# Optimization experiments

Hardware: AMD Instinct MI355X
Metric: run time of the kernel (lower is better)

The kernel has to match this reference:

```python
import jax, jax.numpy as jnp
import numpy as np

B, N, C = 2, 1024, 81          # images, proposals/img, classes (class 0 = background)
H, W = 1024, 1024              # image size
D = 100                        # detections_per_img
WX, WY, WW, WH = 10.0, 10.0, 5.0, 5.0   # BoxCoder weights
SCORE_THRESH = 0.05
NMS_THRESH = 0.5
BBOX_XFORM_CLIP = float(np.log(1000.0 / 16.0))
NEG = -1e30
TO_REMOVE = 1.0


def setup_inputs() -> dict:
    key = jax.random.key(0)
    k1, k2, k3, k4 = jax.random.split(key, 4)
    class_logits = jax.random.normal(k1, (B, N, C), jnp.float32)
    regression_outputs = jax.random.normal(k2, (B, N, C * 4), jnp.float32) * 0.5
    # build valid xyxy proposal boxes inside the image
    cxy = jax.random.uniform(k3, (B, N, 2), jnp.float32, 0.0, W - 1.0)
    wh = jax.random.uniform(k4, (B, N, 2), jnp.float32, 8.0, 256.0)
    x1y1 = jnp.clip(cxy - wh / 2, 0.0, W - 1.0)
    x2y2 = jnp.clip(cxy + wh / 2, 0.0, W - 1.0)
    proposals = jnp.concatenate([x1y1, x2y2], axis=-1)
    return dict(class_logits=class_logits,
                regression_outputs=regression_outputs,
                proposals=proposals)


def decode(rel, props):
    # rel: [N, C, 4], props: [N, 4] xyxy -> decoded per-class boxes [N, C, 4], clipped to image
    widths = props[:, 2] - props[:, 0] + TO_REMOVE   # [N]
    heights = props[:, 3] - props[:, 1] + TO_REMOVE
    ctr_x = props[:, 0] + 0.5 * widths
    ctr_y = props[:, 1] + 0.5 * heights
    dx = rel[..., 0] / WX
    dy = rel[..., 1] / WY
    dw = jnp.minimum(rel[..., 2] / WW, BBOX_XFORM_CLIP)
    dh = jnp.minimum(rel[..., 3] / WH, BBOX_XFORM_CLIP)
    pcx = dx * widths[:, None] + ctr_x[:, None]
    pcy = dy * heights[:, None] + ctr_y[:, None]
    pw = jnp.exp(dw) * widths[:, None]
    ph = jnp.exp(dh) * heights[:, None]
    x1 = pcx - 0.5 * pw
    y1 = pcy - 0.5 * ph
    x2 = pcx + 0.5 * pw - 1.0
    y2 = pcy + 0.5 * ph - 1.0
    # clip_to_image
    x1 = jnp.clip(x1, 0.0, W - TO_REMOVE)
    y1 = jnp.clip(y1, 0.0, H - TO_REMOVE)
    x2 = jnp.clip(x2, 0.0, W - TO_REMOVE)
    y2 = jnp.clip(y2, 0.0, H - TO_REMOVE)
    return jnp.stack([x1, y1, x2, y2], axis=-1)


def pairwise_iou(b):
    # b: [N, 4] -> [N, N]
    area = (b[:, 2] - b[:, 0] + TO_REMOVE) * (b[:, 3] - b[:, 1] + TO_REMOVE)
    lt = jnp.maximum(b[:, None, :2], b[None, :, :2])
    rb = jnp.minimum(b[:, None, 2:], b[None, :, 2:])
    wh = jnp.clip(rb - lt + TO_REMOVE, 0.0)
    inter = wh[..., 0] * wh[..., 1]
    return inter / (area[:, None] + area[None, :] - inter)


def nms_keep(boxes, scores):
    # boxes [N,4], scores [N] (NEG for below-threshold boxes) -> keep mask [N] bool
    order = jnp.argsort(-scores)
    b = boxes[order]
    iou = pairwise_iou(b)                       # [N, N]
    valid = scores[order] > NEG / 2             # below-threshold boxes never participate
    idx = jnp.arange(N)

    def body(i, keep):
        sup = keep[i] & (iou[i] > NMS_THRESH) & (idx > i)
        return keep & ~sup

    keep_sorted = jax.lax.fori_loop(0, N, body, valid)
    return jnp.zeros(N, bool).at[order].set(keep_sorted)


def _per_image(logits, rel, props):
    probs = jax.nn.softmax(logits, axis=-1)                 # [N, C]
    boxes = decode(rel.reshape(N, C, 4), props)             # [N, C, 4]
    cls_boxes = jnp.transpose(boxes[:, 1:, :], (1, 0, 2))   # [C-1, N, 4]  (skip background)
    cls_scores = probs[:, 1:].T                              # [C-1, N]
    valid = cls_scores > SCORE_THRESH
    masked_in = jnp.where(valid, cls_scores, NEG)
    keep = jax.vmap(nms_keep)(cls_boxes, masked_in)          # [C-1, N]
    surv = jnp.where(keep & valid, cls_scores, NEG)
    top_scores, top_idx = jax.lax.top_k(surv.reshape(-1), D)  # over (C-1)*N candidates
    cls_idx = top_idx // N
    box_idx = top_idx % N
    sel_boxes = cls_boxes[cls_idx, box_idx]                  # [D, 4]
    labels = cls_idx + 1
    ok = top_scores > NEG / 2
    return (jnp.where(ok[:, None], sel_boxes, 0.0),
            jnp.where(ok, top_scores, 0.0),
            jnp.where(ok, labels, -1))


def reference(class_logits, regression_outputs, proposals):
    # returns (boxes [B,D,4], scores [B,D], labels [B,D]); invalid slots zeroed / label -1
    return jax.vmap(_per_image)(class_logits, regression_outputs, proposals)
```

## Files before the change

kernel.cpp:

```cpp
#include <hip/hip_runtime.h>
#include <math.h>
#include <float.h>

#define BN 2
#define NP 1024
#define NC 81
#define ND 100
#define MAXC 8192
#define CAP 1024
#define NBIN 4096
#define SCORE_T 0.05f
#define NMS_T 0.5f
#define BBOX_CLIP 4.135166556742356f

__device__ __forceinline__ void decode_box(
    const float* __restrict__ props, const float* __restrict__ regress,
    int b, int n, int c, float& x1, float& y1, float& x2, float& y2)
{
    const float* pr = props + ((size_t)b * NP + n) * 4;
    float p0 = pr[0], p1 = pr[1], p2 = pr[2], p3 = pr[3];
    float w  = p2 - p0 + 1.0f, h = p3 - p1 + 1.0f;
    float cx = p0 + 0.5f * w,  cy = p1 + 0.5f * h;
    const float* rl = regress + (((size_t)b * NP + n) * NC + c) * 4;
    float dx = rl[0] / 10.0f, dy = rl[1] / 10.0f;
    float dw = fminf(rl[2] / 5.0f, BBOX_CLIP);
    float dh = fminf(rl[3] / 5.0f, BBOX_CLIP);
    float pcx = dx * w + cx, pcy = dy * h + cy;
    float pw  = expf(dw) * w, ph = expf(dh) * h;
    x1 = pcx - 0.5f * pw; y1 = pcy - 0.5f * ph;
    x2 = pcx + 0.5f * pw - 1.0f; y2 = pcy + 0.5f * ph - 1.0f;
    x1 = fminf(fmaxf(x1, 0.f), 1023.f);
    y1 = fminf(fmaxf(y1, 0.f), 1023.f);
    x2 = fminf(fmaxf(x2, 0.f), 1023.f);
    y2 = fminf(fmaxf(y2, 0.f), 1023.f);
}

__global__ __launch_bounds__(256) void softmax_probs_kernel(
    const float* __restrict__ logits, float* __restrict__ probs_t, int* __restrict__ cnt)
{
    int g = blockIdx.x * 256 + threadIdx.x;
    if (g == 0) { cnt[0] = 0; cnt[1] = 0; }
    if (g >= BN * NP) return;
    int b = g / NP, n = g % NP;
    const float* row = logits + (size_t)g * NC;
    float m = -FLT_MAX;
    for (int i = 0; i < NC; ++i) m = fmaxf(m, row[i]);
    float s = 0.f;
    for (int i = 0; i < NC; ++i) s += expf(row[i] - m);
    for (int c = 1; c < NC; ++c)
        probs_t[((size_t)b * (NC - 1) + (c - 1)) * NP + n] = expf(row[c] - m) / s;
}

__global__ __launch_bounds__(64) void per_class_nms_kernel(
    const float* __restrict__ probs_t, const float* __restrict__ regress,
    const float* __restrict__ props, int* __restrict__ cnt,
    unsigned long long* __restrict__ g_key)
{
    const int b   = blockIdx.x / (NC - 1);
    const int cls = blockIdx.x % (NC - 1);
    const int c   = cls + 1;
    const int tid = threadIdx.x;

    __shared__ float s_score[NP];
    __shared__ int   s_idx[NP];
    __shared__ float s_x1[NP], s_y1[NP], s_x2[NP], s_y2[NP], s_area[NP];
    __shared__ int   s_keep[NP];
    __shared__ int   s_cnt;

    if (tid == 0) s_cnt = 0;
    __syncthreads();

    const float* prow = probs_t + ((size_t)b * (NC - 1) + cls) * NP;
    for (int n = tid; n < NP; n += 64) {
        float p = prow[n];
        if (p > SCORE_T) {
            int k = atomicAdd(&s_cnt, 1);
            s_score[k] = p;
            s_idx[k]   = n;
        }
    }
    __syncthreads();
    const int M = s_cnt;
    if (M == 0) return;

    int Mp = 1; while (Mp < M) Mp <<= 1;
    for (int i = M + tid; i < Mp; i += 64) { s_score[i] = -FLT_MAX; s_idx[i] = NP + i; }
    __syncthreads();

    for (int k = 2; k <= Mp; k <<= 1) {
        for (int j = k >> 1; j > 0; j >>= 1) {
            for (int i = tid; i < Mp; i += 64) {
                int ixj = i ^ j;
                if (ixj > i) {
                    bool desc = ((i & k) == 0);
                    float si = s_score[i], sj = s_score[ixj];
                    if (desc ? (si < sj) : (si > sj)) {
                        s_score[i] = sj; s_score[ixj] = si;
                        int t = s_idx[i]; s_idx[i] = s_idx[ixj]; s_idx[ixj] = t;
                    }
                }
            }
            __syncthreads();
        }
    }

    for (int i = tid; i < M; i += 64) {
        int n = s_idx[i];
        float x1, y1, x2, y2;
        decode_box(props, regress, b, n, c, x1, y1, x2, y2);
        s_x1[i] = x1; s_y1[i] = y1; s_x2[i] = x2; s_y2[i] = y2;
        s_area[i] = (x2 - x1 + 1.f) * (y2 - y1 + 1.f);
        s_keep[i] = 1;
    }
    __syncthreads();

    for (int i = 0; i < M; ++i) {
        if (s_keep[i]) {
            float x1i = s_x1[i], y1i = s_y1[i], x2i = s_x2[i], y2i = s_y2[i], ai = s_area[i];
            for (int j = i + 1 + tid; j < M; j += 64) {
                float lx = fmaxf(x1i, s_x1[j]);
                float ly = fmaxf(y1i, s_y1[j]);
                float rx = fminf(x2i, s_x2[j]);
                float ry = fminf(y2i, s_y2[j]);
                float wd = fmaxf(rx - lx + 1.f, 0.f);
                float ht = fmaxf(ry - ly + 1.f, 0.f);
                float inter = wd * ht;
                float iou = inter / (ai + s_area[j] - inter);
                if (iou > NMS_T) s_keep[j] = 0;
            }
        }
        __syncthreads();
    }

    for (int i = tid; i < M; i += 64) {
        if (s_keep[i]) {
            int pos = atomicAdd(&cnt[b], 1);
            if (pos < MAXC) {
                unsigned int sb = __float_as_uint(s_score[i]);
                unsigned int f  = (unsigned int)(cls * NP + s_idx[i]);
                g_key[(size_t)b * MAXC + pos] =
                    ((unsigned long long)sb << 32) | (unsigned long long)(0xFFFFFFFFu - f);
            }
        }
    }
}

__device__ __forceinline__ void emit_slot(
    float* __restrict__ out, const float* __restrict__ props,
    const float* __restrict__ regress, int b, int d, unsigned long long key)
{
    float score = __uint_as_float((unsigned int)(key >> 32));
    float* ob = out + ((size_t)b * ND + d) * 4;
    float* os = out + (size_t)BN * ND * 4 + b * ND + d;
    float* ol = out + (size_t)BN * ND * 5 + b * ND + d;
    if (score > 0.f) {
        unsigned int f = 0xFFFFFFFFu - (unsigned int)(key & 0xFFFFFFFFu);
        int cls = f / NP, n = f % NP;
        float x1, y1, x2, y2;
        decode_box(props, regress, b, n, cls + 1, x1, y1, x2, y2);
        ob[0] = x1; ob[1] = y1; ob[2] = x2; ob[3] = y2;
        *os = score;
        *ol = (float)(cls + 1);
    } else {
        ob[0] = 0.f; ob[1] = 0.f; ob[2] = 0.f; ob[3] = 0.f;
        *os = 0.f;
        *ol = -1.f;
    }
}

__global__ __launch_bounds__(256) void topk_kernel(
    const int* __restrict__ cnt, unsigned long long* __restrict__ g_key,
    const float* __restrict__ props, const float* __restrict__ regress,
    float* __restrict__ out)
{
    const int b = blockIdx.x;
    const int tid = threadIdx.x;

    __shared__ int hist[NBIN];
    __shared__ unsigned long long cbuf[CAP];
    __shared__ int s_bstar, s_cnt2;

    int K = cnt[b]; if (K > MAXC) K = MAXC;
    const unsigned long long* keys = g_key + (size_t)b * MAXC;

    for (int i = tid; i < NBIN; i += 256) hist[i] = 0;
    if (tid == 0) s_cnt2 = 0;
    __syncthreads();

    for (int i = tid; i < K; i += 256)
        atomicAdd(&hist[(int)(keys[i] >> 52)], 1);
    __syncthreads();

    if (tid < 64) {
        int l = tid;
        int gs = 0;
        for (int q = 0; q < 64; ++q) gs += hist[l * 64 + q];
        int pre = gs;
        for (int off = 1; off < 64; off <<= 1) {
            int v = __shfl_up(pre, off, 64);
            if (l >= off) pre += v;
        }
        int total = __shfl(pre, 63, 64);
        int S = total - pre + gs;
        unsigned long long ball = __ballot(S >= ND);
        int gstar = ball ? (63 - __clzll((long long)ball)) : 0;
        int Sg = __shfl(S, gstar, 64);
        int Gg = __shfl(gs, gstar, 64);
        int A  = Sg - Gg;
        int h  = hist[gstar * 64 + l];
        int pre2 = h;
        for (int off = 1; off < 64; off <<= 1) {
            int v = __shfl_up(pre2, off, 64);
            if (l >= off) pre2 += v;
        }
        int T = Gg - pre2 + h;
        unsigned long long ball2 = __ballot(A + T >= ND);
        int binin = ball2 ? (63 - __clzll((long long)ball2)) : 0;
        if (l == 0) s_bstar = gstar * 64 + binin;
    }
    __syncthreads();
    const int bstar = s_bstar;

    for (int i = tid; i < K; i += 256) {
        unsigned long long key = keys[i];
        if ((int)(key >> 52) >= bstar) {
            int p = atomicAdd(&s_cnt2, 1);
            if (p < CAP) cbuf[p] = key;
        }
    }
    __syncthreads();
    const int Tt = s_cnt2;

    if (Tt <= CAP) {
        int Tp = 128; while (Tp < Tt) Tp <<= 1;
        for (int i = Tt + tid; i < Tp; i += 256) cbuf[i] = 0ull;
        __syncthreads();
        for (int k = 2; k <= Tp; k <<= 1) {
            for (int j = k >> 1; j > 0; j >>= 1) {
                for (int i = tid; i < Tp; i += 256) {
                    int ixj = i ^ j;
                    if (ixj > i) {
                        bool desc = ((i & k) == 0);
                        unsigned long long a = cbuf[i], c2 = cbuf[ixj];
                        if (desc ? (a < c2) : (a > c2)) { cbuf[i] = c2; cbuf[ixj] = a; }
                    }
                }
                __syncthreads();
            }
        }
        for (int d = tid; d < ND; d += 256)
            emit_slot(out, props, regress, b, d, cbuf[d]);
    } else {
        __shared__ unsigned long long rk[256];
        __shared__ int rp[256];
        for (int d = 0; d < ND; ++d) {
            unsigned long long bk = 0ull; int bp = -1;
            for (int t = tid; t < K; t += 256) {
                unsigned long long k2 = g_key[(size_t)b * MAXC + t];
                if (k2 > bk) { bk = k2; bp = t; }
            }
            rk[tid] = bk; rp[tid] = bp;
            __syncthreads();
            for (int off = 128; off > 0; off >>= 1) {
                if (tid < off && rk[tid + off] > rk[tid]) {
                    rk[tid] = rk[tid + off]; rp[tid] = rp[tid + off];
                }
                __syncthreads();
            }
            if (tid == 0) {
                emit_slot(out, props, regress, b, d, rk[0]);
                if (rp[0] >= 0) g_key[(size_t)b * MAXC + rp[0]] = 0ull;
            }
            __syncthreads();
        }
    }
}

extern "C" void kernel_launch(void* const* d_in, const int* in_sizes, int n_in,
                              void* d_out, int out_size, void* d_ws, size_t ws_size,
                              hipStream_t stream) {
    const float* logits  = (const float*)d_in[0];
    const float* regress = (const float*)d_in[1];
    const float* props   = (const float*)d_in[2];
    float* out = (float*)d_out;

    char* ws = (char*)d_ws;
    int*   cnt     = (int*)  (ws);
    float* probs_t = (float*)(ws + 256);
    unsigned long long* g_key = (unsigned long long*)(ws + 256 + (size_t)BN * (NC - 1) * NP * 4);

    hipLaunchKernelGGL(softmax_probs_kernel, dim3((BN * NP + 255) / 256), dim3(256), 0, stream,
                       logits, probs_t, cnt);
    hipLaunchKernelGGL(per_class_nms_kernel, dim3(BN * (NC - 1)), dim3(64), 0, stream,
                       probs_t, regress, props, cnt, g_key);
    hipLaunchKernelGGL(topk_kernel, dim3(BN), dim3(256), 0, stream,
                       cnt, g_key, props, regress, out);
}
```

Baseline: 118.7 us.

## Fuse per-class NMS and top-k via last-block-done pattern, pack sort keys

Merges the NMS and top-k kernels into one launch: each per-class block does its NMS, then increments a per-image done counter, and the last block for each image runs the histogram and top-k selection. The NMS sort now orders packed 64-bit score/index keys instead of separate score and index arrays. Shared memory is unioned between the two phases, and the softmax kernel caches each row in registers with 64-thread blocks. This removes one launch and its gap. It adds a serial top-k tail run by a single 64-thread block, and it truncates candidates per class at 512, which could drop valid boxes if more pass the threshold.

Result: slower. 124.7 us (+5.1%).

```diff
diff --git a/kernel.cpp b/kernel.cpp
--- a/kernel.cpp
+++ b/kernel.cpp
@@ -7,11 +7,14 @@
 #define NC 81
 #define ND 100
 #define MAXC 8192
-#define CAP 1024
+#define CAP2 512
+#define CAPT 512
 #define NBIN 4096
 #define SCORE_T 0.05f
 #define NMS_T 0.5f
 #define BBOX_CLIP 4.135166556742356f
+
+typedef unsigned long long ull;
 
 __device__ __forceinline__ void decode_box(
     const float* __restrict__ props, const float* __restrict__ regress,
@@ -35,119 +38,9 @@
     y2 = fminf(fmaxf(y2, 0.f), 1023.f);
 }
 
-__global__ __launch_bounds__(256) void softmax_probs_kernel(
-    const float* __restrict__ logits, float* __restrict__ probs_t, int* __restrict__ cnt)
-{
-    int g = blockIdx.x * 256 + threadIdx.x;
-    if (g == 0) { cnt[0] = 0; cnt[1] = 0; }
-    if (g >= BN * NP) return;
-    int b = g / NP, n = g % NP;
-    const float* row = logits + (size_t)g * NC;
-    float m = -FLT_MAX;
-    for (int i = 0; i < NC; ++i) m = fmaxf(m, row[i]);
-    float s = 0.f;
-    for (int i = 0; i < NC; ++i) s += expf(row[i] - m);
-    for (int c = 1; c < NC; ++c)
-        probs_t[((size_t)b * (NC - 1) + (c - 1)) * NP + n] = expf(row[c] - m) / s;
-}
-
-__global__ __launch_bounds__(64) void per_class_nms_kernel(
-    const float* __restrict__ probs_t, const float* __restrict__ regress,
-    const float* __restrict__ props, int* __restrict__ cnt,
-    unsigned long long* __restrict__ g_key)
-{
-    const int b   = blockIdx.x / (NC - 1);
-    const int cls = blockIdx.x % (NC - 1);
-    const int c   = cls + 1;
-    const int tid = threadIdx.x;
-
-    __shared__ float s_score[NP];
-    __shared__ int   s_idx[NP];
-    __shared__ float s_x1[NP], s_y1[NP], s_x2[NP], s_y2[NP], s_area[NP];
-    __shared__ int   s_keep[NP];
-    __shared__ int   s_cnt;
-
-    if (tid == 0) s_cnt = 0;
-    __syncthreads();
-
-    const float* prow = probs_t + ((size_t)b * (NC - 1) + cls) * NP;
-    for (int n = tid; n < NP; n += 64) {
-        float p = prow[n];
-        if (p > SCORE_T) {
-            int k = atomicAdd(&s_cnt, 1);
-            s_score[k] = p;
-            s_idx[k]   = n;
-        }
-    }
-    __syncthreads();
-    const int M = s_cnt;
-    if (M == 0) return;
-
-    int Mp = 1; while (Mp < M) Mp <<= 1;
-    for (int i = M + tid; i < Mp; i += 64) { s_score[i] = -FLT_MAX; s_idx[i] = NP + i; }
-    __syncthreads();
-
-    for (int k = 2; k <= Mp; k <<= 1) {
-        for (int j = k >> 1; j > 0; j >>= 1) {
-            for (int i = tid; i < Mp; i += 64) {
-                int ixj = i ^ j;
-                if (ixj > i) {
-                    bool desc = ((i & k) == 0);
-                    float si = s_score[i], sj = s_score[ixj];
-                    if (desc ? (si < sj) : (si > sj)) {
-                        s_score[i] = sj; s_score[ixj] = si;
-                        int t = s_idx[i]; s_idx[i] = s_idx[ixj]; s_idx[ixj] = t;
-                    }
-                }
-            }
-            __syncthreads();
-        }
-    }
-
-    for (int i = tid; i < M; i += 64) {
-        int n = s_idx[i];
-        float x1, y1, x2, y2;
-        decode_box(props, regress, b, n, c, x1, y1, x2, y2);
-        s_x1[i] = x1; s_y1[i] = y1; s_x2[i] = x2; s_y2[i] = y2;
-        s_area[i] = (x2 - x1 + 1.f) * (y2 - y1 + 1.f);
-        s_keep[i] = 1;
-    }
-    __syncthreads();
-
-    for (int i = 0; i < M; ++i) {
-        if (s_keep[i]) {
-            float x1i = s_x1[i], y1i = s_y1[i], x2i = s_x2[i], y2i = s_y2[i], ai = s_area[i];
-            for (int j = i + 1 + tid; j < M; j += 64) {
-                float lx = fmaxf(x1i, s_x1[j]);
-                float ly = fmaxf(y1i, s_y1[j]);
-                float rx = fminf(x2i, s_x2[j]);
-                float ry = fminf(y2i, s_y2[j]);
-                float wd = fmaxf(rx - lx + 1.f, 0.f);
-                float ht = fmaxf(ry - ly + 1.f, 0.f);
-                float inter = wd * ht;
-                float iou = inter / (ai + s_area[j] - inter);
-                if (iou > NMS_T) s_keep[j] = 0;
-            }
-        }
-        __syncthreads();
-    }
-
-    for (int i = tid; i < M; i += 64) {
-        if (s_keep[i]) {
-            int pos = atomicAdd(&cnt[b], 1);
-            if (pos < MAXC) {
-                unsigned int sb = __float_as_uint(s_score[i]);
-                unsigned int f  = (unsigned int)(cls * NP + s_idx[i]);
-                g_key[(size_t)b * MAXC + pos] =
-                    ((unsigned long long)sb << 32) | (unsigned long long)(0xFFFFFFFFu - f);
-            }
-        }
-    }
-}
-
 __device__ __forceinline__ void emit_slot(
     float* __restrict__ out, const float* __restrict__ props,
-    const float* __restrict__ regress, int b, int d, unsigned long long key)
+    const float* __restrict__ regress, int b, int d, ull key)
 {
     float score = __uint_as_float((unsigned int)(key >> 32));
     float* ob = out + ((size_t)b * ND + d) * 4;
@@ -168,33 +61,158 @@
     }
 }
 
-__global__ __launch_bounds__(256) void topk_kernel(
-    const int* __restrict__ cnt, unsigned long long* __restrict__ g_key,
-    const float* __restrict__ props, const float* __restrict__ regress,
-    float* __restrict__ out)
-{
-    const int b = blockIdx.x;
+__device__ __forceinline__ void bitonic_desc(ull* a, int len, int tid, int nthr)
+{
+    for (int k = 2; k <= len; k <<= 1) {
+        for (int j = k >> 1; j > 0; j >>= 1) {
+            for (int i = tid; i < len; i += nthr) {
+                int ixj = i ^ j;
+                if (ixj > i) {
+                    bool desc = ((i & k) == 0);
+                    ull x = a[i], y = a[ixj];
+                    if (desc ? (x < y) : (x > y)) { a[i] = y; a[ixj] = x; }
+                }
+            }
+            __syncthreads();
+        }
+    }
+}
+
+__global__ __launch_bounds__(64) void softmax_probs_kernel(
+    const float* __restrict__ logits, float* __restrict__ probs_t,
+    int* __restrict__ cnt, int* __restrict__ done)
+{
+    int g = blockIdx.x * 64 + threadIdx.x;
+    if (g == 0) { cnt[0] = 0; cnt[1] = 0; done[0] = 0; done[1] = 0; }
+    if (g >= BN * NP) return;
+    int b = g / NP, n = g % NP;
+    const float* row = logits + (size_t)g * NC;
+    float r[NC];
+    #pragma unroll
+    for (int i = 0; i < NC; ++i) r[i] = row[i];
+    float m = -FLT_MAX;
+    #pragma unroll
+    for (int i = 0; i < NC; ++i) m = fmaxf(m, r[i]);
+    float e[NC];
+    float s = 0.f;
+    #pragma unroll
+    for (int i = 0; i < NC; ++i) { e[i] = expf(r[i] - m); s += e[i]; }
+    #pragma unroll
+    for (int c = 1; c < NC; ++c)
+        probs_t[((size_t)b * (NC - 1) + (c - 1)) * NP + n] = e[c] / s;
+}
+
+__global__ __launch_bounds__(64) void nms_topk_kernel(
+    const float* __restrict__ probs_t, const float* __restrict__ regress,
+    const float* __restrict__ props, int* __restrict__ cnt, int* __restrict__ done,
+    ull* __restrict__ g_key, float* __restrict__ out)
+{
     const int tid = threadIdx.x;
-
-    __shared__ int hist[NBIN];
-    __shared__ unsigned long long cbuf[CAP];
-    __shared__ int s_bstar, s_cnt2;
-
-    int K = cnt[b]; if (K > MAXC) K = MAXC;
-    const unsigned long long* keys = g_key + (size_t)b * MAXC;
-
-    for (int i = tid; i < NBIN; i += 256) hist[i] = 0;
+    const int idx = blockIdx.x;
+    const int b   = idx / (NC - 1);
+    const int cls = idx % (NC - 1);
+    const int c   = cls + 1;
+
+    __shared__ union {
+        struct {
+            ull   key[CAP2];
+            float x1[CAP2], y1[CAP2], x2[CAP2], y2[CAP2], area[CAP2];
+            int   keep[CAP2];
+        } a;
+        struct {
+            int hist[NBIN];
+            ull cbuf[CAPT];
+        } t;
+    } sm;
+    __shared__ int s_cnt, s_ret, s_bstar, s_cnt2;
+
+    if (tid == 0) s_cnt = 0;
+    __syncthreads();
+
+    const float* prow = probs_t + ((size_t)b * (NC - 1) + cls) * NP;
+    for (int n = tid; n < NP; n += 64) {
+        float p = prow[n];
+        if (p > SCORE_T) {
+            int k = atomicAdd(&s_cnt, 1);
+            if (k < CAP2)
+                sm.a.key[k] = ((ull)__float_as_uint(p) << 32)
+                            | (ull)(0xFFFFFFFFu - (unsigned)n);
+        }
+    }
+    __syncthreads();
+    int M = s_cnt; if (M > CAP2) M = CAP2;
+
+    if (M > 0) {
+        int Mp = 2; while (Mp < M) Mp <<= 1;
+        for (int i = M + tid; i < Mp; i += 64) sm.a.key[i] = 0ull;
+        __syncthreads();
+
+        bitonic_desc(sm.a.key, Mp, tid, 64);
+
+        for (int i = tid; i < M; i += 64) {
+            int n = (int)(0xFFFFFFFFu - (unsigned)(sm.a.key[i] & 0xFFFFFFFFu));
+            float x1, y1, x2, y2;
+            decode_box(props, regress, b, n, c, x1, y1, x2, y2);
+            sm.a.x1[i] = x1; sm.a.y1[i] = y1; sm.a.x2[i] = x2; sm.a.y2[i] = y2;
+            sm.a.area[i] = (x2 - x1 + 1.f) * (y2 - y1 + 1.f);
+            sm.a.keep[i] = 1;
+        }
+        __syncthreads();
+
+        for (int i = 0; i < M; ++i) {
+            if (sm.a.keep[i]) {
+                float x1i = sm.a.x1[i], y1i = sm.a.y1[i];
+                float x2i = sm.a.x2[i], y2i = sm.a.y2[i], ai = sm.a.area[i];
+                for (int j = i + 1 + tid; j < M; j += 64) {
+                    float lx = fmaxf(x1i, sm.a.x1[j]);
+                    float ly = fmaxf(y1i, sm.a.y1[j]);
+                    float rx = fminf(x2i, sm.a.x2[j]);
+                    float ry = fminf(y2i, sm.a.y2[j]);
+                    float wd = fmaxf(rx - lx + 1.f, 0.f);
+                    float ht = fmaxf(ry - ly + 1.f, 0.f);
+                    float inter = wd * ht;
+                    float iou = inter / (ai + sm.a.area[j] - inter);
+                    if (iou > NMS_T) sm.a.keep[j] = 0;
+                }
+            }
+            __syncthreads();
+        }
+
+        for (int i = tid; i < M; i += 64) {
+            if (sm.a.keep[i]) {
+                int pos = atomicAdd(&cnt[b], 1);
+                if (pos < MAXC) {
+                    ull key = sm.a.key[i];
+                    unsigned n = 0xFFFFFFFFu - (unsigned)(key & 0xFFFFFFFFu);
+                    unsigned f = (unsigned)cls * NP + n;
+                    g_key[(size_t)b * MAXC + pos] =
+                        (key & 0xFFFFFFFF00000000ull) | (ull)(0xFFFFFFFFu - f);
+                }
+            }
+        }
+    }
+
+    __threadfence();
+    if (tid == 0) s_ret = atomicAdd(&done[b], 1);
+    __syncthreads();
+    if (s_ret != (NC - 1) - 1) return;
+    __threadfence();
+
+    int K = atomicAdd(&cnt[b], 0); if (K > MAXC) K = MAXC;
+    ull* keys = g_key + (size_t)b * MAXC;
+
+    for (int i = tid; i < NBIN; i += 64) sm.t.hist[i] = 0;
     if (tid == 0) s_cnt2 = 0;
     __syncthreads();
 
-    for (int i = tid; i < K; i += 256)
-        atomicAdd(&hist[(int)(keys[i] >> 52)], 1);
-    __syncthreads();
-
-    if (tid < 64) {
+    for (int i = tid; i < K; i += 64)
+        atomicAdd(&sm.t.hist[(int)(keys[i] >> 52)], 1);
+    __syncthreads();
+
+    {
         int l = tid;
         int gs = 0;
-        for (int q = 0; q < 64; ++q) gs += hist[l * 64 + q];
+        for (int q = 0; q < 64; ++q) gs += sm.t.hist[l * 64 + q];
         int pre = gs;
         for (int off = 1; off < 64; off <<= 1) {
             int v = __shfl_up(pre, off, 64);
@@ -202,75 +220,60 @@
         }
         int total = __shfl(pre, 63, 64);
         int S = total - pre + gs;
-        unsigned long long ball = __ballot(S >= ND);
+        ull ball = __ballot(S >= ND);
         int gstar = ball ? (63 - __clzll((long long)ball)) : 0;
         int Sg = __shfl(S, gstar, 64);
         int Gg = __shfl(gs, gstar, 64);
         int A  = Sg - Gg;
-        int h  = hist[gstar * 64 + l];
+        int h  = sm.t.hist[gstar * 64 + l];
         int pre2 = h;
         for (int off = 1; off < 64; off <<= 1) {
             int v = __shfl_up(pre2, off, 64);
             if (l >= off) pre2 += v;
         }
         int T = Gg - pre2 + h;
-        unsigned long long ball2 = __ballot(A + T >= ND);
+        ull ball2 = __ballot(A + T >= ND);
         int binin = ball2 ? (63 - __clzll((long long)ball2)) : 0;
         if (l == 0) s_bstar = gstar * 64 + binin;
     }
     __syncthreads();
     const int bstar = s_bstar;
 
-    for (int i = tid; i < K; i += 256) {
-        unsigned long long key = keys[i];
+    for (int i = tid; i < K; i += 64) {
+        ull key = keys[i];
         if ((int)(key >> 52) >= bstar) {
             int p = atomicAdd(&s_cnt2, 1);
-            if (p < CAP) cbuf[p] = key;
+            if (p < CAPT) sm.t.cbuf[p] = key;
         }
     }
     __syncthreads();
     const int Tt = s_cnt2;
 
-    if (Tt <= CAP) {
+    if (Tt <= CAPT) {
         int Tp = 128; while (Tp < Tt) Tp <<= 1;
-        for (int i = Tt + tid; i < Tp; i += 256) cbuf[i] = 0ull;
+        for (int i = Tt + tid; i < Tp; i += 64) sm.t.cbuf[i] = 0ull;
         __syncthreads();
-        for (int k = 2; k <= Tp; k <<= 1) {
-            for (int j = k >> 1; j > 0; j >>= 1) {
-                for (int i = tid; i < Tp; i += 256) {
-                    int ixj = i ^ j;
-                    if (ixj > i) {
-                        bool desc = ((i & k) == 0);
-                        unsigned long long a = cbuf[i], c2 = cbuf[ixj];
-                        if (desc ? (a < c2) : (a > c2)) { cbuf[i] = c2; cbuf[ixj] = a; }
-                    }
-                }
-                __syncthreads();
-            }
-        }
-        for (int d = tid; d < ND; d += 256)
-            emit_slot(out, props, regress, b, d, cbuf[d]);
+        bitonic_desc(sm.t.cbuf, Tp, tid, 64);
+        for (int d = tid; d < ND; d += 64)
+            emit_slot(out, props, regress, b, d, sm.t.cbuf[d]);
     } else {
-        __shared__ unsigned long long rk[256];
-        __shared__ int rp[256];
         for (int d = 0; d < ND; ++d) {
-            unsigned long long bk = 0ull; int bp = -1;
-            for (int t = tid; t < K; t += 256) {
-                unsigned long long k2 = g_key[(size_t)b * MAXC + t];
+            ull bk = 0ull; int bp = -1;
+            for (int t = tid; t < K; t += 64) {
+                ull k2 = keys[t];
                 if (k2 > bk) { bk = k2; bp = t; }
             }
-            rk[tid] = bk; rp[tid] = bp;
-            __syncthreads();
-            for (int off = 128; off > 0; off >>= 1) {
-                if (tid < off && rk[tid + off] > rk[tid]) {
-                    rk[tid] = rk[tid + off]; rp[tid] = rp[tid + off];
-                }
-                __syncthreads();
-            }
+            for (int off = 32; off > 0; off >>= 1) {
+                ull ok = __shfl_down(bk, off, 64);
+                int op = __shfl_down(bp, off, 64);
+                if (ok > bk) { bk = ok; bp = op; }
+            }
+            bk = __shfl(bk, 0, 64); bp = __shfl(bp, 0, 64);
             if (tid == 0) {
-                emit_slot(out, props, regress, b, d, rk[0]);
-                if (rp[0] >= 0) g_key[(size_t)b * MAXC + rp[0]] = 0ull;
-            }
+                emit_slot(out, props, regress, b, d, bk);
+                if (bp >= 0) keys[bp] = 0ull;
+            }
+            __threadfence();
             __syncthreads();
         }
     }
@@ -286,13 +289,12 @@
 
     char* ws = (char*)d_ws;
     int*   cnt     = (int*)  (ws);
+    int*   done    = (int*)  (ws + 8);
     float* probs_t = (float*)(ws + 256);
-    unsigned long long* g_key = (unsigned long long*)(ws + 256 + (size_t)BN * (NC - 1) * NP * 4);
-
-    hipLaunchKernelGGL(softmax_probs_kernel, dim3((BN * NP + 255) / 256), dim3(256), 0, stream,
-                       logits, probs_t, cnt);
-    hipLaunchKernelGGL(per_class_nms_kernel, dim3(BN * (NC - 1)), dim3(64), 0, stream,
-                       probs_t, regress, props, cnt, g_key);
-    hipLaunchKernelGGL(topk_kernel, dim3(BN), dim3(256), 0, stream,
-                       cnt, g_key, props, regress, out);
-}
+    ull*   g_key   = (ull*)  (ws + 256 + (size_t)BN * (NC - 1) * NP * 4);
+
+    hipLaunchKernelGGL(softmax_probs_kernel, dim3(BN * NP / 64), dim3(64), 0, stream,
+                       logits, probs_t, cnt, done);
+    hipLaunchKernelGGL(nms_topk_kernel, dim3(BN * (NC - 1)), dim3(64), 0, stream,
+                       probs_t, regress, props, cnt, done, g_key, out);
+}
```
